# Kernel optimization log

Measured on AMD Instinct MI355X. Metric: run time of the kernel, lower is better.

Reference implementation:

```python
import jax, jax.numpy as jnp
import numpy as np

B, I, H = 64, 1024, 1024


def setup_inputs() -> dict:
    key = jax.random.key(0)
    ks = jax.random.split(key, 10)
    lim = 1.0 / np.sqrt(H)
    u = lambda k, shape: jax.random.uniform(k, shape, minval=-lim, maxval=lim, dtype=jnp.float32)
    return {
        "input": jax.random.normal(ks[0], (B, I), dtype=jnp.float32),
        "prev_h": 0.1 * jax.random.normal(ks[1], (B, H), dtype=jnp.float32),
        "prev_c": 0.1 * jax.random.normal(ks[2], (B, H, H), dtype=jnp.float32),
        "prev_n": 0.1 * jax.random.normal(ks[3], (B, H), dtype=jnp.float32),
        "if_weights": u(ks[4], (2, I)),
        "o_weights": u(ks[5], (H, I)),
        "kvq_weights": u(ks[6], (3 * H, I)),
        "if_bias": u(ks[7], (2,)),
        "o_bias": u(ks[8], (H,)),
        "kvq_bias": u(ks[9], (3, H)),
    }


def reference(input, prev_h, prev_c, prev_n, if_weights, o_weights, kvq_weights,
              if_bias, o_bias, kvq_bias):
    # Batched mLSTM cell step. prev_h is carried but unused by the math (as in source).
    hid = prev_n.shape[-1]
    # input/forget gates: [B,2] -> exp gates [B,1]
    i_f = input @ if_weights.T + if_bias
    i = jnp.exp(i_f[:, 0:1])
    f = jnp.exp(i_f[:, 1:2])
    # output gate [B,H]
    o = jax.nn.sigmoid(input @ o_weights.T + o_bias)
    # k,v,q projections of the L2-normalized input
    normed = input / jnp.linalg.norm(input, axis=-1, keepdims=True)
    kvq = normed @ kvq_weights.T                       # [B, 3H]
    k, v, q = jnp.split(kvq, 3, axis=-1)
    k = k * (1.0 / jnp.sqrt(jnp.asarray(hid, input.dtype))) + kvq_bias[0]
    v = v + kvq_bias[1]
    q = q + kvq_bias[2]
    # normalizer state and matrix memory update: c = f*prev_c + i*outer(v,k)
    n = f * prev_n + i * k                             # [B, H]
    c = f[:, :, None] * prev_c + (i * v)[:, :, None] * k[:, None, :]  # [B, H, H]
    # readout h = (c @ q) / max(|n.q|, 1), gated by o
    denom = jnp.maximum(jnp.abs(jnp.sum(n * q, axis=-1, keepdims=True)), 1.0)
    h = o * (jnp.einsum('bhk,bk->bh', c, q) / denom)
    return (h, c, n)
```

## Files before the change

### kernel.cpp

```cpp
#include <hip/hip_runtime.h>
#include <math.h>

#define BB 64
#define II 1024
#define HH 1024

typedef float f4 __attribute__((ext_vector_type(4)));

#define WS_I     0
#define WS_F     64
#define WS_INVN  128
#define WS_DENOM 192
#define WS_O     256
#define WS_K     (256 + 65536)
#define WS_V     (256 + 2*65536)
#define WS_Q     (256 + 3*65536)

__global__ __launch_bounds__(64) void k_gates(const float* __restrict__ input,
                                              const float* __restrict__ if_w,
                                              const float* __restrict__ if_b,
                                              float* __restrict__ ws) {
    int b = blockIdx.x;
    int lane = threadIdx.x;
    const float4* x4 = (const float4*)(input + (size_t)b * II);
    const float4* w0 = (const float4*)(if_w);
    const float4* w1 = (const float4*)(if_w + II);
    float d0 = 0.f, d1 = 0.f, ss = 0.f;
#pragma unroll
    for (int j = 0; j < 4; ++j) {
        int idx = lane + j * 64;
        float4 xv = x4[idx];
        float4 a = w0[idx];
        float4 c = w1[idx];
        d0 += xv.x*a.x + xv.y*a.y + xv.z*a.z + xv.w*a.w;
        d1 += xv.x*c.x + xv.y*c.y + xv.z*c.z + xv.w*c.w;
        ss += xv.x*xv.x + xv.y*xv.y + xv.z*xv.z + xv.w*xv.w;
    }
#pragma unroll
    for (int off = 32; off > 0; off >>= 1) {
        d0 += __shfl_xor(d0, off);
        d1 += __shfl_xor(d1, off);
        ss += __shfl_xor(ss, off);
    }
    if (lane == 0) {
        ws[WS_I + b]    = expf(d0 + if_b[0]);
        ws[WS_F + b]    = expf(d1 + if_b[1]);
        ws[WS_INVN + b] = 1.0f / sqrtf(ss);
    }
}

__global__ __launch_bounds__(512) void k_proj(const float* __restrict__ input,
                                              const float* __restrict__ o_w,
                                              const float* __restrict__ kvq_w,
                                              const float* __restrict__ o_b,
                                              const float* __restrict__ kvq_b,
                                              const float* __restrict__ prev_n,
                                              float* __restrict__ ws,
                                              float* __restrict__ n_out) {
    __shared__ float xl[64 * 512];
    float4* xl4 = (float4*)xl;
    const float4* in4 = (const float4*)input;

    int t = threadIdx.x;
    int wave = t >> 6, lane = t & 63;
    int gr0 = blockIdx.x * 16 + wave * 2;
    const float* wb0 = (gr0 < HH) ? (o_w + (size_t)gr0 * II)
                                  : (kvq_w + (size_t)(gr0 - HH) * II);
    const float* wb1 = wb0 + II;

    float acc0 = 0.f, acc1 = 0.f;
    int sw = lane & 7;

    for (int h = 0; h < 2; ++h) {
        if (h) __syncthreads();
#pragma unroll
        for (int j = 0; j < 16; ++j) {
            int e4 = t + j * 512;
            int b  = e4 >> 7;
            int kq = e4 & 127;
            float4 v = in4[b * 256 + h * 128 + kq];
            xl4[b * 128 + (kq ^ (b & 7))] = v;
        }
        __syncthreads();

        const float4* w40 = (const float4*)(wb0 + h * 512);
        const float4* w41 = (const float4*)(wb1 + h * 512);
        const float4* xb  = xl4 + lane * 128;
#pragma unroll 8
        for (int q = 0; q < 128; ++q) {
            float4 xv = xb[q ^ sw];
            float4 w0 = w40[q];
            float4 w1 = w41[q];
            acc0 += w0.x*xv.x + w0.y*xv.y + w0.z*xv.z + w0.w*xv.w;
            acc1 += w1.x*xv.x + w1.y*xv.y + w1.z*xv.z + w1.w*xv.w;
        }
    }

    float invn = ws[WS_INVN + lane];
    float fb   = ws[WS_F + lane];
    float ib   = ws[WS_I + lane];
#pragma unroll
    for (int r = 0; r < 2; ++r) {
        int gr = gr0 + r;
        float d = r ? acc1 : acc0;
        if (gr < HH) {
            ws[WS_O + lane * HH + gr] = 1.0f / (1.0f + expf(-(d + o_b[gr])));
        } else {
            int wk = gr - HH;
            int which = wk >> 10;
            int hh = wk & 1023;
            float dn = d * invn;
            if (which == 0) {
                float kv = dn * 0.03125f + kvq_b[hh];
                ws[WS_K + lane * HH + hh] = kv;
                n_out[lane * HH + hh] = fb * prev_n[lane * HH + hh] + ib * kv;
            } else if (which == 1) {
                ws[WS_V + lane * HH + hh] = dn + kvq_b[HH + hh];
            } else {
                ws[WS_Q + lane * HH + hh] = dn + kvq_b[2 * HH + hh];
            }
        }
    }
}

__global__ __launch_bounds__(256) void k_denom(const float* __restrict__ n_out,
                                               float* __restrict__ ws) {
    int b = blockIdx.x;
    int t = threadIdx.x;
    int wave = t >> 6, lane = t & 63;
    const float* nb = n_out + (size_t)b * HH;
    const float* qb = ws + WS_Q + (size_t)b * HH;
    float s = 0.f;
    for (int idx = t; idx < HH; idx += 256) s += nb[idx] * qb[idx];
#pragma unroll
    for (int off = 32; off > 0; off >>= 1) s += __shfl_xor(s, off);
    __shared__ float red[4];
    if (lane == 0) red[wave] = s;
    __syncthreads();
    if (t == 0) {
        float tot = red[0] + red[1] + red[2] + red[3];
        ws[WS_DENOM + b] = fmaxf(fabsf(tot), 1.0f);
    }
}

__global__ __launch_bounds__(256) void k_cup(const float* __restrict__ prev_c,
                                             const float* __restrict__ ws,
                                             float* __restrict__ c_out,
                                             float* __restrict__ h_out) {
    int wave = threadIdx.x >> 6, lane = threadIdx.x & 63;
    int g0 = (blockIdx.x * 4 + wave) * 4;
    int b = g0 >> 10;
    float fb = ws[WS_F + b], ib = ws[WS_I + b];
    float iv0 = ib * ws[WS_V + g0];
    float iv1 = ib * ws[WS_V + g0 + 1];
    float iv2 = ib * ws[WS_V + g0 + 2];
    float iv3 = ib * ws[WS_V + g0 + 3];
    const f4* pc = (const f4*)(prev_c + ((size_t)g0 << 10));
    f4*       co = (f4*)(c_out + ((size_t)g0 << 10));
    const float4* k4 = (const float4*)(ws + WS_K + (size_t)b * HH);
    const float4* q4 = (const float4*)(ws + WS_Q + (size_t)b * HH);
    float s0 = 0.f, s1 = 0.f, s2 = 0.f, s3 = 0.f;
#pragma unroll
    for (int j = 0; j < 4; ++j) {
        int idx = lane + j * 64;
        float4 kv = k4[idx], qv = q4[idx];
        f4 p, c;
        p = __builtin_nontemporal_load(&pc[idx]);
        c.x = fb*p.x + iv0*kv.x; c.y = fb*p.y + iv0*kv.y;
        c.z = fb*p.z + iv0*kv.z; c.w = fb*p.w + iv0*kv.w;
        __builtin_nontemporal_store(c, &co[idx]);
        s0 += c.x*qv.x + c.y*qv.y + c.z*qv.z + c.w*qv.w;

        p = __builtin_nontemporal_load(&pc[idx + 256]);
        c.x = fb*p.x + iv1*kv.x; c.y = fb*p.y + iv1*kv.y;
        c.z = fb*p.z + iv1*kv.z; c.w = fb*p.w + iv1*kv.w;
        __builtin_nontemporal_store(c, &co[idx + 256]);
        s1 += c.x*qv.x + c.y*qv.y + c.z*qv.z + c.w*qv.w;

        p = __builtin_nontemporal_load(&pc[idx + 512]);
        c.x = fb*p.x + iv2*kv.x; c.y = fb*p.y + iv2*kv.y;
        c.z = fb*p.z + iv2*kv.z; c.w = fb*p.w + iv2*kv.w;
        __builtin_nontemporal_store(c, &co[idx + 512]);
        s2 += c.x*qv.x + c.y*qv.y + c.z*qv.z + c.w*qv.w;

        p = __builtin_nontemporal_load(&pc[idx + 768]);
        c.x = fb*p.x + iv3*kv.x; c.y = fb*p.y + iv3*kv.y;
        c.z = fb*p.z + iv3*kv.z; c.w = fb*p.w + iv3*kv.w;
        __builtin_nontemporal_store(c, &co[idx + 768]);
        s3 += c.x*qv.x + c.y*qv.y + c.z*qv.z + c.w*qv.w;
    }
#pragma unroll
    for (int off = 32; off > 0; off >>= 1) {
        s0 += __shfl_xor(s0, off);
        s1 += __shfl_xor(s1, off);
        s2 += __shfl_xor(s2, off);
        s3 += __shfl_xor(s3, off);
    }
    if (lane == 0) {
        float inv_d = 1.0f / ws[WS_DENOM + b];
        h_out[g0]     = ws[WS_O + g0]     * s0 * inv_d;
        h_out[g0 + 1] = ws[WS_O + g0 + 1] * s1 * inv_d;
        h_out[g0 + 2] = ws[WS_O + g0 + 2] * s2 * inv_d;
        h_out[g0 + 3] = ws[WS_O + g0 + 3] * s3 * inv_d;
    }
}

extern "C" void kernel_launch(void* const* d_in, const int* in_sizes, int n_in,
                              void* d_out, int out_size, void* d_ws, size_t ws_size,
                              hipStream_t stream) {
    const float* input  = (const float*)d_in[0];
    const float* prev_c = (const float*)d_in[2];
    const float* prev_n = (const float*)d_in[3];
    const float* if_w   = (const float*)d_in[4];
    const float* o_w    = (const float*)d_in[5];
    const float* kvq_w  = (const float*)d_in[6];
    const float* if_b   = (const float*)d_in[7];
    const float* o_b    = (const float*)d_in[8];
    const float* kvq_b  = (const float*)d_in[9];

    float* out   = (float*)d_out;
    float* h_out = out;
    float* c_out = out + 65536;
    float* n_out = out + 65536 + 67108864;
    float* ws    = (float*)d_ws;

    k_gates<<<BB, 64, 0, stream>>>(input, if_w, if_b, ws);
    k_proj <<<256, 512, 0, stream>>>(input, o_w, kvq_w, o_b, kvq_b, prev_n, ws, n_out);
    k_denom<<<BB, 256, 0, stream>>>(n_out, ws);
    k_cup  <<<4096, 256, 0, stream>>>(prev_c, ws, c_out, h_out);
}
```

Before: 146.9 us.

## Double-buffer prev_c rows into LDS via async global_load_lds in k_cup

Rewrites the memory-bound c-update kernel so each block handles 32 rows of one batch. It stages k and q once in LDS and streams prev_c through two LDS buffers with async global-to-LDS loads, prefetching the next 4-row chunk while the current one is computed. Output stores switch from nontemporal to regular stores and the grid is halved. The aim is to keep more loads in flight, at the cost of 40KB of LDS per block, lower occupancy and a block barrier per chunk.

```diff
diff --git a/kernel.cpp b/kernel.cpp
--- a/kernel.cpp
+++ b/kernel.cpp
@@ -15,6 +15,12 @@
 #define WS_K     (256 + 65536)
 #define WS_V     (256 + 2*65536)
 #define WS_Q     (256 + 3*65536)
+
+__device__ __forceinline__ void gll16(const float* g, float* l) {
+    __builtin_amdgcn_global_load_lds(
+        (const __attribute__((address_space(1))) unsigned int*)g,
+        (__attribute__((address_space(3))) unsigned int*)l, 16, 0, 0);
+}
 
 __global__ __launch_bounds__(64) void k_gates(const float* __restrict__ input,
                                               const float* __restrict__ if_w,
@@ -147,61 +153,65 @@
                                              const float* __restrict__ ws,
                                              float* __restrict__ c_out,
                                              float* __restrict__ h_out) {
-    int wave = threadIdx.x >> 6, lane = threadIdx.x & 63;
-    int g0 = (blockIdx.x * 4 + wave) * 4;
-    int b = g0 >> 10;
+    __shared__ float kq[2048];
+    __shared__ float cbuf[2][4096];
+
+    int t = threadIdx.x;
+    int wave = t >> 6, lane = t & 63;
+    int b = blockIdx.x >> 5;
+    int r0 = (blockIdx.x & 31) << 5;
+    size_t gbase = ((size_t)b << 20) + ((size_t)r0 << 10);
+
+    const float* kp = ws + WS_K + (size_t)b * HH;
+    const float* qp = ws + WS_Q + (size_t)b * HH;
+
+    gll16(kp + 4 * t, kq + 4 * t);
+    gll16(qp + 4 * t, kq + 1024 + 4 * t);
+#pragma unroll
+    for (int i = 0; i < 4; ++i) {
+        int slot = t + i * 256;
+        gll16(prev_c + gbase + 4 * slot, cbuf[0] + 4 * slot);
+    }
+    __syncthreads();
+
     float fb = ws[WS_F + b], ib = ws[WS_I + b];
-    float iv0 = ib * ws[WS_V + g0];
-    float iv1 = ib * ws[WS_V + g0 + 1];
-    float iv2 = ib * ws[WS_V + g0 + 2];
-    float iv3 = ib * ws[WS_V + g0 + 3];
-    const f4* pc = (const f4*)(prev_c + ((size_t)g0 << 10));
-    f4*       co = (f4*)(c_out + ((size_t)g0 << 10));
-    const float4* k4 = (const float4*)(ws + WS_K + (size_t)b * HH);
-    const float4* q4 = (const float4*)(ws + WS_Q + (size_t)b * HH);
-    float s0 = 0.f, s1 = 0.f, s2 = 0.f, s3 = 0.f;
-#pragma unroll
-    for (int j = 0; j < 4; ++j) {
-        int idx = lane + j * 64;
-        float4 kv = k4[idx], qv = q4[idx];
-        f4 p, c;
-        p = __builtin_nontemporal_load(&pc[idx]);
-        c.x = fb*p.x + iv0*kv.x; c.y = fb*p.y + iv0*kv.y;
-        c.z = fb*p.z + iv0*kv.z; c.w = fb*p.w + iv0*kv.w;
-        __builtin_nontemporal_store(c, &co[idx]);
-        s0 += c.x*qv.x + c.y*qv.y + c.z*qv.z + c.w*qv.w;
-
-        p = __builtin_nontemporal_load(&pc[idx + 256]);
-        c.x = fb*p.x + iv1*kv.x; c.y = fb*p.y + iv1*kv.y;
-        c.z = fb*p.z + iv1*kv.z; c.w = fb*p.w + iv1*kv.w;
-        __builtin_nontemporal_store(c, &co[idx + 256]);
-        s1 += c.x*qv.x + c.y*qv.y + c.z*qv.z + c.w*qv.w;
-
-        p = __builtin_nontemporal_load(&pc[idx + 512]);
-        c.x = fb*p.x + iv2*kv.x; c.y = fb*p.y + iv2*kv.y;
-        c.z = fb*p.z + iv2*kv.z; c.w = fb*p.w + iv2*kv.w;
-        __builtin_nontemporal_store(c, &co[idx + 512]);
-        s2 += c.x*qv.x + c.y*qv.y + c.z*qv.z + c.w*qv.w;
-
-        p = __builtin_nontemporal_load(&pc[idx + 768]);
-        c.x = fb*p.x + iv3*kv.x; c.y = fb*p.y + iv3*kv.y;
-        c.z = fb*p.z + iv3*kv.z; c.w = fb*p.w + iv3*kv.w;
-        __builtin_nontemporal_store(c, &co[idx + 768]);
-        s3 += c.x*qv.x + c.y*qv.y + c.z*qv.z + c.w*qv.w;
-    }
-#pragma unroll
-    for (int off = 32; off > 0; off >>= 1) {
-        s0 += __shfl_xor(s0, off);
-        s1 += __shfl_xor(s1, off);
-        s2 += __shfl_xor(s2, off);
-        s3 += __shfl_xor(s3, off);
-    }
-    if (lane == 0) {
-        float inv_d = 1.0f / ws[WS_DENOM + b];
-        h_out[g0]     = ws[WS_O + g0]     * s0 * inv_d;
-        h_out[g0 + 1] = ws[WS_O + g0 + 1] * s1 * inv_d;
-        h_out[g0 + 2] = ws[WS_O + g0 + 2] * s2 * inv_d;
-        h_out[g0 + 3] = ws[WS_O + g0 + 3] * s3 * inv_d;
+    float inv_d = 1.0f / ws[WS_DENOM + b];
+
+    int buf = 0;
+    for (int tc = 0; tc < 8; ++tc) {
+        if (tc < 7) {
+            const float* src = prev_c + gbase + ((size_t)(tc + 1) << 12);
+#pragma unroll
+            for (int i = 0; i < 4; ++i) {
+                int slot = t + i * 256;
+                gll16(src + 4 * slot, cbuf[buf ^ 1] + 4 * slot);
+            }
+        }
+        int g = (b << 10) + r0 + (tc << 2) + wave;
+        float iv = ib * ws[WS_V + g];
+        float og = ws[WS_O + g];
+        const f4* pr = (const f4*)(cbuf[buf]) + wave * 256;
+        const f4* k4 = (const f4*)kq;
+        const f4* q4 = (const f4*)kq + 256;
+        f4* co = (f4*)(c_out + ((size_t)g << 10));
+        float s = 0.f;
+#pragma unroll
+        for (int j = 0; j < 4; ++j) {
+            int idx = lane + j * 64;
+            f4 p = pr[idx], kv = k4[idx], qv = q4[idx];
+            f4 c;
+            c.x = fb * p.x + iv * kv.x;
+            c.y = fb * p.y + iv * kv.y;
+            c.z = fb * p.z + iv * kv.z;
+            c.w = fb * p.w + iv * kv.w;
+            co[idx] = c;
+            s += c.x * qv.x + c.y * qv.y + c.z * qv.z + c.w * qv.w;
+        }
+#pragma unroll
+        for (int off = 32; off > 0; off >>= 1) s += __shfl_xor(s, off);
+        if (lane == 0) h_out[g] = og * s * inv_d;
+        __syncthreads();
+        buf ^= 1;
     }
 }
 
@@ -227,5 +237,5 @@
     k_gates<<<BB, 64, 0, stream>>>(input, if_w, if_b, ws);
     k_proj <<<256, 512, 0, stream>>>(input, o_w, kvq_w, o_b, kvq_b, prev_n, ws, n_out);
     k_denom<<<BB, 256, 0, stream>>>(n_out, ws);
-    k_cup  <<<4096, 256, 0, stream>>>(prev_c, ws, c_out, h_out);
-}
+    k_cup  <<<2048, 256, 0, stream>>>(prev_c, ws, c_out, h_out);
+}
```

New measurement: 162.7 us. 1.11x slower.

## Split K across waves in projection kernel, keep input slice in registers

Applied to the files above, without the earlier changes.

The projection kernel no longer stages the whole input batch in 128KB of shared memory. Each wave now holds a 128-wide K slice of one batch row's input in registers and walks all 16 output rows of the block, writing partial sums to a small LDS buffer that is reduced after a single barrier. This removes the large LDS footprint and the per-half barriers so that more blocks can be resident, requested via launch_bounds(512,2). The cost is 128 VGPRs of input per thread, which risks spills or low occupancy, and weight loads are now broadcast across lanes.

```diff
diff --git a/kernel.cpp b/kernel.cpp
--- a/kernel.cpp
+++ b/kernel.cpp
@@ -49,60 +49,50 @@
     }
 }
 
-__global__ __launch_bounds__(512) void k_proj(const float* __restrict__ input,
-                                              const float* __restrict__ o_w,
-                                              const float* __restrict__ kvq_w,
-                                              const float* __restrict__ o_b,
-                                              const float* __restrict__ kvq_b,
-                                              const float* __restrict__ prev_n,
-                                              float* __restrict__ ws,
-                                              float* __restrict__ n_out) {
-    __shared__ float xl[64 * 512];
-    float4* xl4 = (float4*)xl;
-    const float4* in4 = (const float4*)input;
+__global__ __launch_bounds__(512, 2) void k_proj(const float* __restrict__ input,
+                                                 const float* __restrict__ o_w,
+                                                 const float* __restrict__ kvq_w,
+                                                 const float* __restrict__ o_b,
+                                                 const float* __restrict__ kvq_b,
+                                                 const float* __restrict__ prev_n,
+                                                 float* __restrict__ ws,
+                                                 float* __restrict__ n_out) {
+    __shared__ float pl[16 * 512];
 
     int t = threadIdx.x;
-    int wave = t >> 6, lane = t & 63;
-    int gr0 = blockIdx.x * 16 + wave * 2;
-    const float* wb0 = (gr0 < HH) ? (o_w + (size_t)gr0 * II)
-                                  : (kvq_w + (size_t)(gr0 - HH) * II);
-    const float* wb1 = wb0 + II;
-
-    float acc0 = 0.f, acc1 = 0.f;
-    int sw = lane & 7;
-
-    for (int h = 0; h < 2; ++h) {
-        if (h) __syncthreads();
-#pragma unroll
-        for (int j = 0; j < 16; ++j) {
-            int e4 = t + j * 512;
-            int b  = e4 >> 7;
-            int kq = e4 & 127;
-            float4 v = in4[b * 256 + h * 128 + kq];
-            xl4[b * 128 + (kq ^ (b & 7))] = v;
+    int w = t >> 6, lane = t & 63;
+    int rbase = blockIdx.x * 16;
+
+    const f4* xs = (const f4*)(input + (size_t)lane * II + w * 128);
+    f4 xr[32];
+#pragma unroll
+    for (int q = 0; q < 32; ++q) xr[q] = xs[q];
+
+    for (int r = 0; r < 16; ++r) {
+        int gr = rbase + r;
+        const float* wrow = (gr < HH) ? (o_w + (size_t)gr * II)
+                                      : (kvq_w + (size_t)(gr - HH) * II);
+        const f4* w4 = (const f4*)(wrow + w * 128);
+        float acc = 0.f;
+#pragma unroll
+        for (int q = 0; q < 32; ++q) {
+            f4 wv = w4[q];
+            acc += wv.x*xr[q].x + wv.y*xr[q].y + wv.z*xr[q].z + wv.w*xr[q].w;
         }
-        __syncthreads();
-
-        const float4* w40 = (const float4*)(wb0 + h * 512);
-        const float4* w41 = (const float4*)(wb1 + h * 512);
-        const float4* xb  = xl4 + lane * 128;
-#pragma unroll 8
-        for (int q = 0; q < 128; ++q) {
-            float4 xv = xb[q ^ sw];
-            float4 w0 = w40[q];
-            float4 w1 = w41[q];
-            acc0 += w0.x*xv.x + w0.y*xv.y + w0.z*xv.z + w0.w*xv.w;
-            acc1 += w1.x*xv.x + w1.y*xv.y + w1.z*xv.z + w1.w*xv.w;
-        }
-    }
+        pl[r * 512 + w * 64 + lane] = acc;
+    }
+    __syncthreads();
 
     float invn = ws[WS_INVN + lane];
     float fb   = ws[WS_F + lane];
     float ib   = ws[WS_I + lane];
 #pragma unroll
-    for (int r = 0; r < 2; ++r) {
-        int gr = gr0 + r;
-        float d = r ? acc1 : acc0;
+    for (int rr = 0; rr < 2; ++rr) {
+        int r  = 2 * w + rr;
+        int gr = rbase + r;
+        float d = 0.f;
+#pragma unroll
+        for (int j = 0; j < 8; ++j) d += pl[r * 512 + j * 64 + lane];
         if (gr < HH) {
             ws[WS_O + lane * HH + gr] = 1.0f / (1.0f + expf(-(d + o_b[gr])));
         } else {
```

Measured after the change: 150.9 us. 1.03x slower.
